# Kernel tuning notes

Measured on AMD Instinct MI355X. Metric: run time of the kernel, lower is better.

The kernel has to match this reference:

```python
import jax, jax.numpy as jnp
import numpy as np
from jax import lax

B, T, IN, H = 4096, 512, 11, 16


def lstm(x, Wih, Whh, bih, bhh):
    # x: [B, T, in]; PyTorch gate order i, f, g, o packed along 4H.
    xg = jnp.einsum('bti,gi->btg', x, Wih) + bih + bhh  # [B, T, 4H]
    h0 = jnp.zeros((x.shape[0], Whh.shape[1]), x.dtype)
    c0 = jnp.zeros_like(h0)

    def step(carry, xg_t):
        h, c = carry
        g = xg_t + h @ Whh.T                      # [B, 4H]
        i, f, gg, o = jnp.split(g, 4, axis=-1)
        i = jax.nn.sigmoid(i)
        f = jax.nn.sigmoid(f)
        gg = jnp.tanh(gg)
        o = jax.nn.sigmoid(o)
        c = f * c + i * gg
        h = o * jnp.tanh(c)
        return (h, c), h

    _, hs = lax.scan(step, (h0, c0), jnp.swapaxes(xg, 0, 1))  # hs: [T, B, H]
    return jnp.swapaxes(hs, 0, 1)  # [B, T, H]


def setup_inputs() -> dict:
    key = jax.random.key(0)
    ks = jax.random.split(key, 16)
    s = 1.0 / np.sqrt(H)
    u = lambda k, shape: jax.random.uniform(k, shape, jnp.float32, -s, s)
    return {
        'x': jax.random.normal(ks[0], (B, T, IN), jnp.float32),
        'Wih1': u(ks[1], (4 * H, IN)), 'Whh1': u(ks[2], (4 * H, H)),
        'bih1': u(ks[3], (4 * H,)), 'bhh1': u(ks[4], (4 * H,)),
        'Wih2': u(ks[5], (4 * H, H)), 'Whh2': u(ks[6], (4 * H, H)),
        'bih2': u(ks[7], (4 * H,)), 'bhh2': u(ks[8], (4 * H,)),
        'Wd1': u(ks[9], (8, H)), 'bd1': u(ks[10], (8,)),
        'Wd2': u(ks[11], (8, 8)), 'bd2': u(ks[12], (8,)),
        'Wd3': u(ks[13], (3, 8)), 'bd3': u(ks[14], (3,)),
    }


def reference(x, Wih1, Whh1, bih1, bhh1, Wih2, Whh2, bih2, bhh2,
              Wd1, bd1, Wd2, bd2, Wd3, bd3):
    h1 = lstm(x, Wih1, Whh1, bih1, bhh1)          # [B, T, H]
    # Dropout2d treated as identity (eval mode).
    h2 = lstm(h1, Wih2, Whh2, bih2, bhh2)          # [B, T, H]
    s = jax.nn.softmax(h2, axis=1)[:, -1, :]       # softmax over TIME, take last step -> [B, H]
    d = (s @ Wd1.T + bd1) @ Wd2.T + bd2
    d = d @ Wd3.T + bd3                            # [B, 3]
    return jax.nn.softmax(d, axis=1)
```

## Files before the change

kernel.cpp:

```cpp
#include <hip/hip_runtime.h>

#define T_STEPS 512
#define IN_DIM 11
#define H_DIM 16
#define ROW_F (T_STEPS * IN_DIM)
#define LOG2E 1.44269504088896340736f

typedef float v2f __attribute__((ext_vector_type(2)));
typedef float v4f __attribute__((ext_vector_type(4)));

__device__ __forceinline__ v2f pk_fma(v2f a, v2f b, v2f c) {
    v2f d;
    asm("v_pk_fma_f32 %0, %1, %2, %3" : "=v"(d) : "v"(a), "v"(b), "v"(c));
    return d;
}

template<int CTRL>
__device__ __forceinline__ float qperm(float v) {
    return __builtin_bit_cast(float,
        __builtin_amdgcn_update_dpp(0, __builtin_bit_cast(int, v),
                                    CTRL, 0xf, 0xf, true));
}

__device__ __forceinline__ float bcast_lane(float v, int l) {
    return __builtin_bit_cast(float,
        __builtin_amdgcn_readlane(__builtin_bit_cast(int, v), l));
}

#define ACT_STEP(gsum, cst, hv_out)                                           \
    {                                                                         \
        const float a_ = __builtin_fmaf(vAa,                                  \
            __builtin_amdgcn_rcpf(1.0f + __builtin_amdgcn_exp2f(gsum)), vBc); \
        const float gi_ = qperm<0x00>(a_);                                    \
        const float gf_ = qperm<0x55>(a_);                                    \
        const float gg_ = qperm<0xAA>(a_);                                    \
        const float go_ = qperm<0xFF>(a_);                                    \
        cst = __builtin_fmaf(gf_, cst, gi_ * gg_);                            \
        const float tc_ = __builtin_fmaf(2.0f,                                \
            __builtin_amdgcn_rcpf(1.0f +                                      \
                __builtin_amdgcn_exp2f(-2.0f * LOG2E * cst)), -1.0f);         \
        hv_out = go_ * tc_;                                                   \
    }

__global__ __launch_bounds__(256, 4) void lstm2_head(
    const float* __restrict__ x,
    const float* __restrict__ Wih1, const float* __restrict__ Whh1,
    const float* __restrict__ bih1, const float* __restrict__ bhh1,
    const float* __restrict__ Wih2, const float* __restrict__ Whh2,
    const float* __restrict__ bih2, const float* __restrict__ bhh2,
    const float* __restrict__ Wd1, const float* __restrict__ bd1,
    const float* __restrict__ Wd2, const float* __restrict__ bd2,
    const float* __restrict__ Wd3, const float* __restrict__ bd3,
    float* __restrict__ out)
{
    __shared__ alignas(16) float shh[4][2][H_DIM];

    const int lane = threadIdx.x & 63;
    const int wid = __builtin_amdgcn_readfirstlane((int)(threadIdx.x >> 6));
    const int b = blockIdx.x * 4 + wid;

    const int r   = lane >> 2;
    const int gt  = lane & 3;
    const int row = gt * H_DIM + r;

    const bool is_t = (gt == 2);
    const float M   = is_t ? (-2.0f * LOG2E) : (-LOG2E);
    const float vAa = is_t ? 2.0f : 1.0f;
    const float vBc = is_t ? -1.0f : 0.0f;

    float wx[IN_DIM];
    #pragma unroll
    for (int k = 0; k < IN_DIM; ++k) wx[k] = M * Wih1[row * IN_DIM + k];
    v2f wh1p[8], wi2p[8], wh2p[8];
    #pragma unroll
    for (int j = 0; j < 8; ++j) {
        wh1p[j] = (v2f){M * Whh1[row * H_DIM + 2 * j], M * Whh1[row * H_DIM + 2 * j + 1]};
        wi2p[j] = (v2f){M * Wih2[row * H_DIM + 2 * j], M * Wih2[row * H_DIM + 2 * j + 1]};
        wh2p[j] = (v2f){M * Whh2[row * H_DIM + 2 * j], M * Whh2[row * H_DIM + 2 * j + 1]};
    }
    const float bb1 = M * (bih1[row] + bhh1[row]);
    const float bb2 = M * (bih2[row] + bhh2[row]);
    #pragma unroll
    for (int k = 0; k < IN_DIM; ++k) asm volatile("" : "+v"(wx[k]));
    #pragma unroll
    for (int j = 0; j < 8; ++j) {
        asm volatile("" : "+v"(wh1p[j]));
        asm volatile("" : "+v"(wi2p[j]));
        asm volatile("" : "+v"(wh2p[j]));
    }

    float* const hs1 = &shh[wid][0][0];
    float* const hs2 = &shh[wid][1][0];
    const v4f* const h1q4 = (const v4f*)hs1;
    const v4f* const h2q4 = (const v4f*)hs2;
    hs1[r] = 0.0f;
    hs2[r] = 0.0f;

    const float* __restrict__ xb = x + (size_t)b * ROW_F;

    float c1 = 0.f, c2 = 0.f, h2v = 0.f, ssum = 0.f;
    v2f h1r[8], h2r[8];
    #pragma unroll
    for (int j = 0; j < 8; ++j) { h1r[j] = (v2f){0.f, 0.f}; h2r[j] = (v2f){0.f, 0.f}; }

    #pragma unroll 8
    for (int t = 0; t < T_STEPS; ++t) {
        const float* __restrict__ xr = xb + t * IN_DIM;

        float xs0 = __builtin_fmaf(wx[0], xr[0], bb1);
        float xs1 = wx[1] * xr[1];
        xs0 = __builtin_fmaf(wx[2], xr[2], xs0);
        xs1 = __builtin_fmaf(wx[3], xr[3], xs1);
        xs0 = __builtin_fmaf(wx[4], xr[4], xs0);
        xs1 = __builtin_fmaf(wx[5], xr[5], xs1);
        xs0 = __builtin_fmaf(wx[6], xr[6], xs0);
        xs1 = __builtin_fmaf(wx[7], xr[7], xs1);
        xs0 = __builtin_fmaf(wx[8], xr[8], xs0);
        xs1 = __builtin_fmaf(wx[9], xr[9], xs1);
        xs0 = __builtin_fmaf(wx[10], xr[10], xs0);

        v2f a2p = pk_fma(wh2p[0], h2r[0], (v2f){bb2, 0.f});
        v2f a2q = pk_fma(wh2p[1], h2r[1], (v2f){0.f, 0.f});
        #pragma unroll
        for (int j = 2; j < 8; j += 2) {
            a2p = pk_fma(wh2p[j],     h2r[j],     a2p);
            a2q = pk_fma(wh2p[j + 1], h2r[j + 1], a2q);
        }

        v2f a1p = pk_fma(wh1p[0], h1r[0], (v2f){xs0, xs1});
        v2f a1q = pk_fma(wh1p[1], h1r[1], (v2f){0.f, 0.f});
        #pragma unroll
        for (int j = 2; j < 8; j += 2) {
            a1p = pk_fma(wh1p[j],     h1r[j],     a1p);
            a1q = pk_fma(wh1p[j + 1], h1r[j + 1], a1q);
        }

        const v2f s1 = a1p + a1q;
        const float g1 = s1.x + s1.y;
        float h1v;
        ACT_STEP(g1, c1, h1v);
        hs1[r] = h1v;
        #pragma unroll
        for (int j = 0; j < 4; ++j) {
            const v4f q = h1q4[j];
            h1r[2 * j]     = (v2f){q.x, q.y};
            h1r[2 * j + 1] = (v2f){q.z, q.w};
        }

        #pragma unroll
        for (int j = 0; j < 8; j += 2) {
            a2p = pk_fma(wi2p[j],     h1r[j],     a2p);
            a2q = pk_fma(wi2p[j + 1], h1r[j + 1], a2q);
        }

        const v2f s2 = a2p + a2q;
        const float g2 = s2.x + s2.y;
        ACT_STEP(g2, c2, h2v);
        hs2[r] = h2v;
        #pragma unroll
        for (int j = 0; j < 4; ++j) {
            const v4f q = h2q4[j];
            h2r[2 * j]     = (v2f){q.x, q.y};
            h2r[2 * j + 1] = (v2f){q.z, q.w};
        }

        ssum += __builtin_amdgcn_exp2f(LOG2E * h2v);
    }

    const float sv = __builtin_amdgcn_exp2f(LOG2E * h2v) / ssum;

    float ssb[H_DIM];
    #pragma unroll
    for (int k = 0; k < H_DIM; ++k) ssb[k] = bcast_lane(sv, 4 * k);

    const int r8 = lane & 7;
    float acc1 = bd1[r8];
    #pragma unroll
    for (int k = 0; k < H_DIM; ++k)
        acc1 = __builtin_fmaf(Wd1[r8 * H_DIM + k], ssb[k], acc1);

    float d1s[8];
    #pragma unroll
    for (int j = 0; j < 8; ++j) d1s[j] = bcast_lane(acc1, j);

    float acc2 = bd2[r8];
    #pragma unroll
    for (int k = 0; k < 8; ++k)
        acc2 = __builtin_fmaf(Wd2[r8 * 8 + k], d1s[k], acc2);

    float d2s[8];
    #pragma unroll
    for (int j = 0; j < 8; ++j) d2s[j] = bcast_lane(acc2, j);

    float lg = 0.f;
    if (lane < 3) {
        lg = bd3[lane];
        #pragma unroll
        for (int k = 0; k < 8; ++k)
            lg = __builtin_fmaf(Wd3[lane * 8 + k], d2s[k], lg);
    }
    const float l0 = bcast_lane(lg, 0);
    const float l1 = bcast_lane(lg, 1);
    const float l2 = bcast_lane(lg, 2);
    const float mx = fmaxf(l0, fmaxf(l1, l2));
    const float e0 = __builtin_amdgcn_exp2f(LOG2E * (l0 - mx));
    const float e1 = __builtin_amdgcn_exp2f(LOG2E * (l1 - mx));
    const float e2 = __builtin_amdgcn_exp2f(LOG2E * (l2 - mx));
    const float inv = 1.0f / (e0 + e1 + e2);
    if (lane < 3) {
        const float ev = (lane == 0) ? e0 : ((lane == 1) ? e1 : e2);
        out[b * 3 + lane] = ev * inv;
    }
}

extern "C" void kernel_launch(void* const* d_in, const int* in_sizes, int n_in,
                              void* d_out, int out_size, void* d_ws, size_t ws_size,
                              hipStream_t stream) {
    (void)in_sizes; (void)n_in; (void)out_size; (void)d_ws; (void)ws_size;
    const float* x    = (const float*)d_in[0];
    const float* Wih1 = (const float*)d_in[1];
    const float* Whh1 = (const float*)d_in[2];
    const float* bih1 = (const float*)d_in[3];
    const float* bhh1 = (const float*)d_in[4];
    const float* Wih2 = (const float*)d_in[5];
    const float* Whh2 = (const float*)d_in[6];
    const float* bih2 = (const float*)d_in[7];
    const float* bhh2 = (const float*)d_in[8];
    const float* Wd1  = (const float*)d_in[9];
    const float* bd1  = (const float*)d_in[10];
    const float* Wd2  = (const float*)d_in[11];
    const float* bd2  = (const float*)d_in[12];
    const float* Wd3  = (const float*)d_in[13];
    const float* bd3  = (const float*)d_in[14];

    lstm2_head<<<dim3(4096 / 4), dim3(256), 0, stream>>>(
        x, Wih1, Whh1, bih1, bhh1, Wih2, Whh2, bih2, bhh2,
        Wd1, bd1, Wd2, bd2, Wd3, bd3, (float*)d_out);
}
```

Measured before the change: 505.7 us.

## Interleave two batch rows per wave and stage x chunks through LDS

Result: no change. 499.3 us (-1.3%).

```diff
diff --git a/kernel.cpp b/kernel.cpp
--- a/kernel.cpp
+++ b/kernel.cpp
@@ -2,8 +2,13 @@
 
 #define T_STEPS 512
 #define IN_DIM 11
+#define ROW_PAD 12
 #define H_DIM 16
 #define ROW_F (T_STEPS * IN_DIM)
+#define CHUNK_T 16
+#define CHUNK_F (CHUNK_T * IN_DIM)
+#define N_CHUNK (T_STEPS / CHUNK_T)
+#define NB 2
 #define LOG2E 1.44269504088896340736f
 
 typedef float v2f __attribute__((ext_vector_type(2)));
@@ -42,7 +47,7 @@
         hv_out = go_ * tc_;                                                   \
     }
 
-__global__ __launch_bounds__(256, 4) void lstm2_head(
+__global__ __launch_bounds__(256, 2) void lstm2_head(
     const float* __restrict__ x,
     const float* __restrict__ Wih1, const float* __restrict__ Whh1,
     const float* __restrict__ bih1, const float* __restrict__ bhh1,
@@ -53,11 +58,12 @@
     const float* __restrict__ Wd3, const float* __restrict__ bd3,
     float* __restrict__ out)
 {
-    __shared__ alignas(16) float shh[4][2][H_DIM];
+    __shared__ alignas(16) float xlds[4][NB][2][212];
+    __shared__ alignas(16) float shh[4][NB][2][H_DIM];
 
     const int lane = threadIdx.x & 63;
     const int wid = __builtin_amdgcn_readfirstlane((int)(threadIdx.x >> 6));
-    const int b = blockIdx.x * 4 + wid;
+    const int b0 = blockIdx.x * (4 * NB) + wid * NB;
 
     const int r   = lane >> 2;
     const int gt  = lane & 3;
@@ -68,10 +74,11 @@
     const float vAa = is_t ? 2.0f : 1.0f;
     const float vBc = is_t ? -1.0f : 0.0f;
 
-    float wx[IN_DIM];
-    #pragma unroll
-    for (int k = 0; k < IN_DIM; ++k) wx[k] = M * Wih1[row * IN_DIM + k];
-    v2f wh1p[8], wi2p[8], wh2p[8];
+    v2f wi1p[6], wh1p[8], wi2p[8], wh2p[8];
+    #pragma unroll
+    for (int j = 0; j < 5; ++j)
+        wi1p[j] = (v2f){M * Wih1[row * IN_DIM + 2 * j], M * Wih1[row * IN_DIM + 2 * j + 1]};
+    wi1p[5] = (v2f){M * Wih1[row * IN_DIM + 10], 0.0f};
     #pragma unroll
     for (int j = 0; j < 8; ++j) {
         wh1p[j] = (v2f){M * Whh1[row * H_DIM + 2 * j], M * Whh1[row * H_DIM + 2 * j + 1]};
@@ -81,7 +88,7 @@
     const float bb1 = M * (bih1[row] + bhh1[row]);
     const float bb2 = M * (bih2[row] + bhh2[row]);
     #pragma unroll
-    for (int k = 0; k < IN_DIM; ++k) asm volatile("" : "+v"(wx[k]));
+    for (int j = 0; j < 6; ++j) asm volatile("" : "+v"(wi1p[j]));
     #pragma unroll
     for (int j = 0; j < 8; ++j) {
         asm volatile("" : "+v"(wh1p[j]));
@@ -89,127 +96,196 @@
         asm volatile("" : "+v"(wh2p[j]));
     }
 
-    float* const hs1 = &shh[wid][0][0];
-    float* const hs2 = &shh[wid][1][0];
-    const v4f* const h1q4 = (const v4f*)hs1;
-    const v4f* const h2q4 = (const v4f*)hs2;
-    hs1[r] = 0.0f;
-    hs2[r] = 0.0f;
-
-    const float* __restrict__ xb = x + (size_t)b * ROW_F;
-
-    float c1 = 0.f, c2 = 0.f, h2v = 0.f, ssum = 0.f;
-    v2f h1r[8], h2r[8];
-    #pragma unroll
-    for (int j = 0; j < 8; ++j) { h1r[j] = (v2f){0.f, 0.f}; h2r[j] = (v2f){0.f, 0.f}; }
-
-    #pragma unroll 8
-    for (int t = 0; t < T_STEPS; ++t) {
-        const float* __restrict__ xr = xb + t * IN_DIM;
-
-        float xs0 = __builtin_fmaf(wx[0], xr[0], bb1);
-        float xs1 = wx[1] * xr[1];
-        xs0 = __builtin_fmaf(wx[2], xr[2], xs0);
-        xs1 = __builtin_fmaf(wx[3], xr[3], xs1);
-        xs0 = __builtin_fmaf(wx[4], xr[4], xs0);
-        xs1 = __builtin_fmaf(wx[5], xr[5], xs1);
-        xs0 = __builtin_fmaf(wx[6], xr[6], xs0);
-        xs1 = __builtin_fmaf(wx[7], xr[7], xs1);
-        xs0 = __builtin_fmaf(wx[8], xr[8], xs0);
-        xs1 = __builtin_fmaf(wx[9], xr[9], xs1);
-        xs0 = __builtin_fmaf(wx[10], xr[10], xs0);
-
-        v2f a2p = pk_fma(wh2p[0], h2r[0], (v2f){bb2, 0.f});
-        v2f a2q = pk_fma(wh2p[1], h2r[1], (v2f){0.f, 0.f});
-        #pragma unroll
-        for (int j = 2; j < 8; j += 2) {
-            a2p = pk_fma(wh2p[j],     h2r[j],     a2p);
-            a2q = pk_fma(wh2p[j + 1], h2r[j + 1], a2q);
-        }
-
-        v2f a1p = pk_fma(wh1p[0], h1r[0], (v2f){xs0, xs1});
-        v2f a1q = pk_fma(wh1p[1], h1r[1], (v2f){0.f, 0.f});
-        #pragma unroll
-        for (int j = 2; j < 8; j += 2) {
-            a1p = pk_fma(wh1p[j],     h1r[j],     a1p);
-            a1q = pk_fma(wh1p[j + 1], h1r[j + 1], a1q);
-        }
-
-        const v2f s1 = a1p + a1q;
-        const float g1 = s1.x + s1.y;
-        float h1v;
-        ACT_STEP(g1, c1, h1v);
-        hs1[r] = h1v;
-        #pragma unroll
-        for (int j = 0; j < 4; ++j) {
-            const v4f q = h1q4[j];
-            h1r[2 * j]     = (v2f){q.x, q.y};
-            h1r[2 * j + 1] = (v2f){q.z, q.w};
-        }
-
-        #pragma unroll
-        for (int j = 0; j < 8; j += 2) {
-            a2p = pk_fma(wi2p[j],     h1r[j],     a2p);
-            a2q = pk_fma(wi2p[j + 1], h1r[j + 1], a2q);
-        }
-
-        const v2f s2 = a2p + a2q;
-        const float g2 = s2.x + s2.y;
-        ACT_STEP(g2, c2, h2v);
-        hs2[r] = h2v;
-        #pragma unroll
-        for (int j = 0; j < 4; ++j) {
-            const v4f q = h2q4[j];
-            h2r[2 * j]     = (v2f){q.x, q.y};
-            h2r[2 * j + 1] = (v2f){q.z, q.w};
-        }
-
-        ssum += __builtin_amdgcn_exp2f(LOG2E * h2v);
-    }
-
-    const float sv = __builtin_amdgcn_exp2f(LOG2E * h2v) / ssum;
-
-    float ssb[H_DIM];
-    #pragma unroll
-    for (int k = 0; k < H_DIM; ++k) ssb[k] = bcast_lane(sv, 4 * k);
-
-    const int r8 = lane & 7;
-    float acc1 = bd1[r8];
-    #pragma unroll
-    for (int k = 0; k < H_DIM; ++k)
-        acc1 = __builtin_fmaf(Wd1[r8 * H_DIM + k], ssb[k], acc1);
-
-    float d1s[8];
-    #pragma unroll
-    for (int j = 0; j < 8; ++j) d1s[j] = bcast_lane(acc1, j);
-
-    float acc2 = bd2[r8];
-    #pragma unroll
-    for (int k = 0; k < 8; ++k)
-        acc2 = __builtin_fmaf(Wd2[r8 * 8 + k], d1s[k], acc2);
-
-    float d2s[8];
-    #pragma unroll
-    for (int j = 0; j < 8; ++j) d2s[j] = bcast_lane(acc2, j);
-
-    float lg = 0.f;
-    if (lane < 3) {
-        lg = bd3[lane];
+    const float* __restrict__ xb[NB];
+    #pragma unroll
+    for (int bi = 0; bi < NB; ++bi) xb[bi] = x + (size_t)(b0 + bi) * ROW_F;
+
+    float* hs1[NB]; float* hs2[NB];
+    const v4f* h1q4[NB]; const v4f* h2q4[NB];
+    #pragma unroll
+    for (int bi = 0; bi < NB; ++bi) {
+        hs1[bi] = &shh[wid][bi][0][0];
+        hs2[bi] = &shh[wid][bi][1][0];
+        h1q4[bi] = (const v4f*)hs1[bi];
+        h2q4[bi] = (const v4f*)hs2[bi];
+    }
+
+    if (lane < 32) {
+        const int buf = lane >> 4, rr = lane & 15;
+        xlds[wid][0][buf][rr * ROW_PAD + IN_DIM] = 0.0f;
+        xlds[wid][1][buf][rr * ROW_PAD + IN_DIM] = 0.0f;
+    }
+
+    const int f1i = lane, f2i = lane + 64, f3i = lane + 128;
+    const int p1 = (f1i / IN_DIM) * ROW_PAD + (f1i % IN_DIM);
+    const int p2 = (f2i / IN_DIM) * ROW_PAD + (f2i % IN_DIM);
+    const int p3 = (f3i / IN_DIM) * ROW_PAD + (f3i % IN_DIM);
+
+    float gl0[NB], gl1[NB], gl2[NB];
+    #pragma unroll
+    for (int bi = 0; bi < NB; ++bi) {
+        gl0[bi] = xb[bi][f1i];
+        gl1[bi] = xb[bi][f2i];
+        gl2[bi] = xb[bi][min(f3i, ROW_F - 1)];
+    }
+
+    float c1[NB], c2[NB], h2v[NB], ssum[NB];
+    v2f h1r[NB][8], h2r[NB][8];
+    #pragma unroll
+    for (int bi = 0; bi < NB; ++bi) {
+        c1[bi] = 0.f; c2[bi] = 0.f; h2v[bi] = 0.f; ssum[bi] = 0.f;
+        #pragma unroll
+        for (int j = 0; j < 8; ++j) {
+            h1r[bi][j] = (v2f){0.f, 0.f};
+            h2r[bi][j] = (v2f){0.f, 0.f};
+        }
+    }
+
+    for (int ck = 0; ck < N_CHUNK; ++ck) {
+        float* xbuf[NB];
+        #pragma unroll
+        for (int bi = 0; bi < NB; ++bi) {
+            xbuf[bi] = &xlds[wid][bi][ck & 1][0];
+            xbuf[bi][p1] = gl0[bi];
+            xbuf[bi][p2] = gl1[bi];
+            xbuf[bi][p3] = gl2[bi];
+        }
+        if (ck + 1 < N_CHUNK) {
+            const int base = (ck + 1) * CHUNK_F;
+            #pragma unroll
+            for (int bi = 0; bi < NB; ++bi) {
+                gl0[bi] = xb[bi][base + f1i];
+                gl1[bi] = xb[bi][base + f2i];
+                gl2[bi] = xb[bi][min(base + f3i, ROW_F - 1)];
+            }
+        }
+
+        #pragma unroll
+        for (int t2 = 0; t2 < CHUNK_T; ++t2) {
+            v2f a2p[NB], a2q[NB], a1p[NB], a1q[NB];
+
+            #pragma unroll
+            for (int bi = 0; bi < NB; ++bi) {
+                a2p[bi] = pk_fma(wh2p[0], h2r[bi][0], (v2f){bb2, 0.f});
+                a2q[bi] = pk_fma(wh2p[1], h2r[bi][1], (v2f){0.f, 0.f});
+                #pragma unroll
+                for (int j = 2; j < 8; j += 2) {
+                    a2p[bi] = pk_fma(wh2p[j],     h2r[bi][j],     a2p[bi]);
+                    a2q[bi] = pk_fma(wh2p[j + 1], h2r[bi][j + 1], a2q[bi]);
+                }
+            }
+
+            #pragma unroll
+            for (int bi = 0; bi < NB; ++bi) {
+                const v2f* const xr = (const v2f*)(xbuf[bi] + t2 * ROW_PAD);
+                a1p[bi] = pk_fma(wi1p[0], xr[0], (v2f){bb1, 0.f});
+                a1q[bi] = pk_fma(wi1p[1], xr[1], (v2f){0.f, 0.f});
+                #pragma unroll
+                for (int j = 2; j < 6; j += 2) {
+                    a1p[bi] = pk_fma(wi1p[j],     xr[j],     a1p[bi]);
+                    a1q[bi] = pk_fma(wi1p[j + 1], xr[j + 1], a1q[bi]);
+                }
+                #pragma unroll
+                for (int j = 0; j < 8; j += 2) {
+                    a1p[bi] = pk_fma(wh1p[j],     h1r[bi][j],     a1p[bi]);
+                    a1q[bi] = pk_fma(wh1p[j + 1], h1r[bi][j + 1], a1q[bi]);
+                }
+            }
+
+            float h1v[NB];
+            #pragma unroll
+            for (int bi = 0; bi < NB; ++bi) {
+                const v2f s1 = a1p[bi] + a1q[bi];
+                const float g1 = s1.x + s1.y;
+                ACT_STEP(g1, c1[bi], h1v[bi]);
+                hs1[bi][r] = h1v[bi];
+            }
+            #pragma unroll
+            for (int bi = 0; bi < NB; ++bi) {
+                #pragma unroll
+                for (int j = 0; j < 4; ++j) {
+                    const v4f q = h1q4[bi][j];
+                    h1r[bi][2 * j]     = (v2f){q.x, q.y};
+                    h1r[bi][2 * j + 1] = (v2f){q.z, q.w};
+                }
+            }
+
+            #pragma unroll
+            for (int bi = 0; bi < NB; ++bi) {
+                #pragma unroll
+                for (int j = 0; j < 8; j += 2) {
+                    a2p[bi] = pk_fma(wi2p[j],     h1r[bi][j],     a2p[bi]);
+                    a2q[bi] = pk_fma(wi2p[j + 1], h1r[bi][j + 1], a2q[bi]);
+                }
+            }
+
+            #pragma unroll
+            for (int bi = 0; bi < NB; ++bi) {
+                const v2f s2 = a2p[bi] + a2q[bi];
+                const float g2 = s2.x + s2.y;
+                ACT_STEP(g2, c2[bi], h2v[bi]);
+                hs2[bi][r] = h2v[bi];
+            }
+            #pragma unroll
+            for (int bi = 0; bi < NB; ++bi) {
+                #pragma unroll
+                for (int j = 0; j < 4; ++j) {
+                    const v4f q = h2q4[bi][j];
+                    h2r[bi][2 * j]     = (v2f){q.x, q.y};
+                    h2r[bi][2 * j + 1] = (v2f){q.z, q.w};
+                }
+                ssum[bi] += __builtin_amdgcn_exp2f(LOG2E * h2v[bi]);
+            }
+        }
+    }
+
+    #pragma unroll
+    for (int bi = 0; bi < NB; ++bi) {
+        const int b = b0 + bi;
+        const float sv = __builtin_amdgcn_exp2f(LOG2E * h2v[bi]) / ssum[bi];
+
+        float ssb[H_DIM];
+        #pragma unroll
+        for (int k = 0; k < H_DIM; ++k) ssb[k] = bcast_lane(sv, 4 * k);
+
+        const int r8 = lane & 7;
+        float acc1 = bd1[r8];
+        #pragma unroll
+        for (int k = 0; k < H_DIM; ++k)
+            acc1 = __builtin_fmaf(Wd1[r8 * H_DIM + k], ssb[k], acc1);
+
+        float d1s[8];
+        #pragma unroll
+        for (int j = 0; j < 8; ++j) d1s[j] = bcast_lane(acc1, j);
+
+        float acc2 = bd2[r8];
         #pragma unroll
         for (int k = 0; k < 8; ++k)
-            lg = __builtin_fmaf(Wd3[lane * 8 + k], d2s[k], lg);
-    }
-    const float l0 = bcast_lane(lg, 0);
-    const float l1 = bcast_lane(lg, 1);
-    const float l2 = bcast_lane(lg, 2);
-    const float mx = fmaxf(l0, fmaxf(l1, l2));
-    const float e0 = __builtin_amdgcn_exp2f(LOG2E * (l0 - mx));
-    const float e1 = __builtin_amdgcn_exp2f(LOG2E * (l1 - mx));
-    const float e2 = __builtin_amdgcn_exp2f(LOG2E * (l2 - mx));
-    const float inv = 1.0f / (e0 + e1 + e2);
-    if (lane < 3) {
-        const float ev = (lane == 0) ? e0 : ((lane == 1) ? e1 : e2);
-        out[b * 3 + lane] = ev * inv;
+            acc2 = __builtin_fmaf(Wd2[r8 * 8 + k], d1s[k], acc2);
+
+        float d2s[8];
+        #pragma unroll
+        for (int j = 0; j < 8; ++j) d2s[j] = bcast_lane(acc2, j);
+
+        float lg = 0.f;
+        if (lane < 3) {
+            lg = bd3[lane];
+            #pragma unroll
+            for (int k = 0; k < 8; ++k)
+                lg = __builtin_fmaf(Wd3[lane * 8 + k], d2s[k], lg);
+        }
+        const float l0 = bcast_lane(lg, 0);
+        const float l1 = bcast_lane(lg, 1);
+        const float l2 = bcast_lane(lg, 2);
+        const float mx = fmaxf(l0, fmaxf(l1, l2));
+        const float e0 = __builtin_amdgcn_exp2f(LOG2E * (l0 - mx));
+        const float e1 = __builtin_amdgcn_exp2f(LOG2E * (l1 - mx));
+        const float e2 = __builtin_amdgcn_exp2f(LOG2E * (l2 - mx));
+        const float inv = 1.0f / (e0 + e1 + e2);
+        if (lane < 3) {
+            const float ev = (lane == 0) ? e0 : ((lane == 1) ? e1 : e2);
+            out[b * 3 + lane] = ev * inv;
+        }
     }
 }
 
@@ -233,7 +309,7 @@
     const float* Wd3  = (const float*)d_in[13];
     const float* bd3  = (const float*)d_in[14];
 
-    lstm2_head<<<dim3(4096 / 4), dim3(256), 0, stream>>>(
+    lstm2_head<<<dim3(4096 / (4 * NB)), dim3(256), 0, stream>>>(
         x, Wih1, Whh1, bih1, bhh1, Wih2, Whh2, bih2, bhh2,
         Wd1, bd1, Wd2, bd2, Wd3, bd3, (float*)d_out);
 }
```
